# Kernel tuning notes

Measured on AMD Instinct MI355X. Metric: run time of the kernel, lower is better.

## Reference

```python
import jax, jax.numpy as jnp
import numpy as np

N, IN_DIM, OUT_DIM, HEADS, SUB = 4096, 256, 128, 4, 32
ETA = 0.5
LAMBDA_SPARSE = 0.05
NEG_BIG = -1e9


def setup_inputs() -> dict:
    key = jax.random.key(0)
    k1, k2, k3, k4 = jax.random.split(key, 4)
    H = jax.random.normal(k1, (N, IN_DIM), dtype=jnp.float32)
    # sparse binary adjacency mask (avg degree ~ 41) with self-loops
    adj_mask = (jax.random.uniform(k2, (N, N)) < 0.01).astype(jnp.float32)
    adj_mask = adj_mask.at[jnp.arange(N), jnp.arange(N)].set(1.0)
    # per-head orthonormal subspace bases U_k = QR(randn)[:, :SUB]
    raw = jax.random.normal(k3, (HEADS, IN_DIM, SUB), dtype=jnp.float32)
    U = jax.vmap(lambda r: jnp.linalg.qr(r)[0])(raw)  # [h, D, s]
    threshold = jnp.full((OUT_DIM,), LAMBDA_SPARSE, dtype=jnp.float32)
    proj_w = jax.random.normal(k4, (OUT_DIM, IN_DIM), dtype=jnp.float32) / np.float32(np.sqrt(IN_DIM))
    return {"H": H, "adj_mask": adj_mask, "U": U, "threshold": threshold, "proj_w": proj_w}


def reference(H, adj_mask, U, threshold, proj_w):
    # Z_k = U_k^T @ H^T  -> [h, s, N]
    Z = jnp.einsum('hds,nd->hsn', U, H)
    # scores_k = Z_k^T @ Z_k / sqrt(s)  -> [h, N, N]
    scores = jnp.einsum('hsn,hsm->hnm', Z, Z) / jnp.sqrt(jnp.float32(SUB))
    scores = scores + (1.0 - adj_mask)[None, :, :] * NEG_BIG
    alpha = jax.nn.softmax(scores, axis=-1)  # torch softmax(dim=1) on [N,N] rows
    # agg_k = Z_k @ alpha_k^T  -> [h, s, N];  sum_k U_k @ agg_k -> [D, N]
    agg = jnp.einsum('hsj,hij->hsi', Z, alpha)
    agg_sum = jnp.einsum('hds,hsn->dn', U, agg)
    H_half = H + ETA * agg_sum.T           # [N, D]
    H_half = H_half @ proj_w.T             # [N, out_dim]
    # soft-threshold
    H_out = jnp.sign(H_half) * jax.nn.relu(jnp.abs(H_half) - threshold[None, :])
    # orthogonality loss: sum_k ||U_k^T U_k - I||_F^2 + sum_{k<l} ||U_k^T U_l||_F^2
    G = jnp.einsum('kds,ldt->klst', U, U)  # [h, h, s, s]
    eye_s = jnp.eye(SUB, dtype=U.dtype)
    eye_h = jnp.eye(HEADS, dtype=U.dtype)
    sub = G - eye_h[:, :, None, None] * eye_s[None, None, :, :]
    sq = jnp.sum(sub ** 2, axis=(2, 3))    # [h, h]
    orth_loss = jnp.sum(jnp.triu(jnp.ones((HEADS, HEADS), dtype=U.dtype)) * sq)
    return H_out, orth_loss
```

## Files before the change

### kernel.cpp

```cpp
#include <hip/hip_runtime.h>
#include <hip/hip_bf16.h>
#include <math.h>

#define NN 4096
#define IN_DIM 256
#define OUT_DIM 128
#define HEADS 4
#define SUB 32
#define MAXDEG 128
#define ETA 0.5f
#define INV_SQRT_SUB 0.17677669529663687f

__global__ __launch_bounds__(256) void fused_small(const float* __restrict__ U,
                                                   const float* __restrict__ PW,
                                                   float* __restrict__ Wcomb,
                                                   float* __restrict__ W2,
                                                   float* __restrict__ loss) {
    int b = blockIdx.x;
    int t = threadIdx.x;
    __shared__ float sh[260];

    if (b < 256) {
        float v;
        if (b < 128) {
            int h = b >> 5, s = b & 31;
            v = U[h * IN_DIM * SUB + t * SUB + s];
        } else {
            v = PW[(b - 128) * IN_DIM + t];
        }
        Wcomb[b * IN_DIM + t] = v;
    } else if (b < 384) {
        int hs = b - 256;
        int h = hs >> 5, s = hs & 31;
        sh[t] = U[h * IN_DIM * SUB + t * SUB + s];
        __syncthreads();
        if (t < 128) {
            const float4* pw4 = (const float4*)(PW + t * IN_DIM);
            const float4* u4  = (const float4*)sh;
            float acc = 0.f;
            #pragma unroll 4
            for (int d4 = 0; d4 < 64; ++d4) {
                float4 a = u4[d4], p = pw4[d4];
                acc += a.x * p.x + a.y * p.y + a.z * p.z + a.w * p.w;
            }
            W2[hs * OUT_DIM + t] = acc;
        }
    } else {
        const int pk[10] = {0,0,0,0,1,1,1,2,2,3};
        const int pl[10] = {0,1,2,3,1,2,3,2,3,3};
        int p = b - 384;
        int k = pk[p], l = pl[p];
        int t2 = t & 31;
        int sg = t >> 5;
        const float* Uk = U + k * IN_DIM * SUB;
        const float* Ul = U + l * IN_DIM * SUB;
        float a0 = 0.f, a1 = 0.f, a2 = 0.f, a3 = 0.f;
        #pragma unroll 4
        for (int d = 0; d < IN_DIM; ++d) {
            float ul = Ul[d * SUB + t2];
            float u0 = Uk[d * SUB + sg * 4 + 0];
            float u1 = Uk[d * SUB + sg * 4 + 1];
            float u2 = Uk[d * SUB + sg * 4 + 2];
            float u3 = Uk[d * SUB + sg * 4 + 3];
            a0 += u0 * ul; a1 += u1 * ul; a2 += u2 * ul; a3 += u3 * ul;
        }
        if (k == l) {
            if (sg * 4 + 0 == t2) a0 -= 1.f;
            if (sg * 4 + 1 == t2) a1 -= 1.f;
            if (sg * 4 + 2 == t2) a2 -= 1.f;
            if (sg * 4 + 3 == t2) a3 -= 1.f;
        }
        float local = a0 * a0 + a1 * a1 + a2 * a2 + a3 * a3;
        local += __shfl_xor(local, 32, 64);
        local += __shfl_xor(local, 16, 64);
        local += __shfl_xor(local, 8, 64);
        local += __shfl_xor(local, 4, 64);
        local += __shfl_xor(local, 2, 64);
        local += __shfl_xor(local, 1, 64);
        if ((t & 63) == 0) sh[256 + (t >> 6)] = local;
        __syncthreads();
        if (t == 0) atomicAdd(loss, sh[256] + sh[257] + sh[258] + sh[259]);
    }
}

#define RPB 8
__global__ __launch_bounds__(256) void compute_zt_p(const float* __restrict__ H,
                                                    const float* __restrict__ Wcomb,
                                                    float* __restrict__ ZT,
                                                    float* __restrict__ P) {
    int t = threadIdx.x;
    int r0 = blockIdx.x * RPB;
    __shared__ float Hs[RPB][IN_DIM];
    const float4* H4 = (const float4*)(H + (size_t)r0 * IN_DIM);
    float4* Hs4 = (float4*)&Hs[0][0];
    Hs4[t]       = H4[t];
    Hs4[t + 256] = H4[t + 256];
    __syncthreads();

    float acc[RPB];
    #pragma unroll
    for (int r = 0; r < RPB; ++r) acc[r] = 0.f;

    const float4* Wr = (const float4*)(Wcomb + t * IN_DIM);
    float4 w = Wr[0];
    #pragma unroll 4
    for (int d4 = 0; d4 < 64; ++d4) {
        float4 wn = Wr[(d4 + 1 < 64) ? d4 + 1 : 63];
        #pragma unroll
        for (int r = 0; r < RPB; ++r) {
            float4 h = *(const float4*)&Hs[r][d4 * 4];
            acc[r] += h.x * w.x + h.y * w.y + h.z * w.z + h.w * w.w;
        }
        w = wn;
    }
    #pragma unroll
    for (int r = 0; r < RPB; ++r) {
        if (t < 128) ZT[(size_t)(r0 + r) * 128 + t] = acc[r];
        else         P [(size_t)(r0 + r) * 128 + (t - 128)] = acc[r];
    }
}

__global__ __launch_bounds__(128) void attn_core(const float* __restrict__ ZT,
                                                 const float* __restrict__ adj,
                                                 float* __restrict__ agg) {
    int i = blockIdx.x;
    int t = threadIdx.x;
    __shared__ int nbr_s[MAXDEG];
    __shared__ int cnt;
    if (t == 0) cnt = 0;
    __syncthreads();

    const float4* row4 = (const float4*)(adj + (size_t)i * NN);
    #pragma unroll
    for (int k2 = 0; k2 < NN / (128 * 4); ++k2) {
        float4 v = row4[t + k2 * 128];
        int j0 = (t + k2 * 128) * 4;
        if (v.x > 0.5f) { int p = atomicAdd(&cnt, 1); if (p < MAXDEG) nbr_s[p] = j0; }
        if (v.y > 0.5f) { int p = atomicAdd(&cnt, 1); if (p < MAXDEG) nbr_s[p] = j0 + 1; }
        if (v.z > 0.5f) { int p = atomicAdd(&cnt, 1); if (p < MAXDEG) nbr_s[p] = j0 + 2; }
        if (v.w > 0.5f) { int p = atomicAdd(&cnt, 1); if (p < MAXDEG) nbr_s[p] = j0 + 3; }
    }
    __syncthreads();
    int dg = cnt < MAXDEG ? cnt : MAXDEG;

    float q = ZT[(size_t)i * 128 + t];
    float accV = 0.f, accS = 0.f;

    for (int jj = 0; jj < dg; jj += 4) {
        int i0 = nbr_s[jj];
        int i1 = nbr_s[(jj + 1 < dg) ? jj + 1 : jj];
        int i2 = nbr_s[(jj + 2 < dg) ? jj + 2 : jj];
        int i3 = nbr_s[(jj + 3 < dg) ? jj + 3 : jj];
        float v0 = ZT[(size_t)i0 * 128 + t];
        float v1 = ZT[(size_t)i1 * 128 + t];
        float v2 = ZT[(size_t)i2 * 128 + t];
        float v3 = ZT[(size_t)i3 * 128 + t];
        float p0 = q * v0, p1 = q * v1, p2 = q * v2, p3 = q * v3;
        p0 += __shfl_xor(p0, 16, 32); p1 += __shfl_xor(p1, 16, 32);
        p2 += __shfl_xor(p2, 16, 32); p3 += __shfl_xor(p3, 16, 32);
        p0 += __shfl_xor(p0, 8, 32);  p1 += __shfl_xor(p1, 8, 32);
        p2 += __shfl_xor(p2, 8, 32);  p3 += __shfl_xor(p3, 8, 32);
        p0 += __shfl_xor(p0, 4, 32);  p1 += __shfl_xor(p1, 4, 32);
        p2 += __shfl_xor(p2, 4, 32);  p3 += __shfl_xor(p3, 4, 32);
        p0 += __shfl_xor(p0, 2, 32);  p1 += __shfl_xor(p1, 2, 32);
        p2 += __shfl_xor(p2, 2, 32);  p3 += __shfl_xor(p3, 2, 32);
        p0 += __shfl_xor(p0, 1, 32);  p1 += __shfl_xor(p1, 1, 32);
        p2 += __shfl_xor(p2, 1, 32);  p3 += __shfl_xor(p3, 1, 32);
        float e0 = __expf(p0 * INV_SQRT_SUB);
        float e1 = (jj + 1 < dg) ? __expf(p1 * INV_SQRT_SUB) : 0.f;
        float e2 = (jj + 2 < dg) ? __expf(p2 * INV_SQRT_SUB) : 0.f;
        float e3 = (jj + 3 < dg) ? __expf(p3 * INV_SQRT_SUB) : 0.f;
        accV += e0 * v0 + e1 * v1 + e2 * v2 + e3 * v3;
        accS += e0 + e1 + e2 + e3;
    }
    agg[(size_t)i * 128 + t] = accV * (ETA / accS);
}

#define EROWS 16
__global__ __launch_bounds__(256) void epilogue(const float* __restrict__ Pm,
                                                const float* __restrict__ agg,
                                                const float* __restrict__ W2,
                                                const float* __restrict__ threshold,
                                                float* __restrict__ out) {
    int t = threadIdx.x;
    int o = t & 127, half = t >> 7;
    int r0 = blockIdx.x * EROWS;
    __shared__ float As[EROWS][128];
    const float4* a4 = (const float4*)(agg + (size_t)r0 * 128);
    float4* As4 = (float4*)&As[0][0];
    As4[t]       = a4[t];
    As4[t + 256] = a4[t + 256];
    __syncthreads();

    float acc[8];
    #pragma unroll
    for (int r = 0; r < 8; ++r) acc[r] = 0.f;

    for (int q4 = 0; q4 < 32; ++q4) {
        int hs = q4 * 4;
        float w0 = W2[(hs + 0) * 128 + o];
        float w1 = W2[(hs + 1) * 128 + o];
        float w2v = W2[(hs + 2) * 128 + o];
        float w3 = W2[(hs + 3) * 128 + o];
        #pragma unroll
        for (int r = 0; r < 8; ++r) {
            float4 a = *(const float4*)&As[half * 8 + r][hs];
            acc[r] += a.x * w0 + a.y * w1 + a.z * w2v + a.w * w3;
        }
    }
    float th = threshold[o];
    #pragma unroll
    for (int r = 0; r < 8; ++r) {
        int row = r0 + half * 8 + r;
        float val = Pm[(size_t)row * 128 + o] + acc[r];
        float av = fabsf(val) - th;
        out[(size_t)row * 128 + o] = (av > 0.f) ? copysignf(av, val) : 0.f;
    }
}

extern "C" void kernel_launch(void* const* d_in, const int* in_sizes, int n_in,
                              void* d_out, int out_size, void* d_ws, size_t ws_size,
                              hipStream_t stream) {
    const float* H   = (const float*)d_in[0];
    const float* adj = (const float*)d_in[1];
    const float* U   = (const float*)d_in[2];
    const float* thr = (const float*)d_in[3];
    const float* PW  = (const float*)d_in[4];
    float* out = (float*)d_out;
    float* loss = out + (size_t)NN * OUT_DIM;

    char* ws = (char*)d_ws;
    float* ZT    = (float*)(ws);
    float* P     = (float*)(ws + (size_t)2097152);
    float* agg   = (float*)(ws + (size_t)4194304);
    float* W2    = (float*)(ws + (size_t)6291456);
    float* Wcomb = (float*)(ws + (size_t)6356992);

    hipMemsetAsync(loss, 0, sizeof(float), stream);
    fused_small<<<394, 256, 0, stream>>>(U, PW, Wcomb, W2, loss);
    compute_zt_p<<<NN / RPB, 256, 0, stream>>>(H, Wcomb, ZT, P);
    attn_core<<<NN, 128, 0, stream>>>(ZT, adj, agg);
    epilogue<<<NN / EROWS, 256, 0, stream>>>(P, agg, W2, thr, out);
}
```

Before: 169.6 us.

## Overlap adjacency scan with projection GEMM and fuse attention with epilogue

The adjacency-row scan now runs in its own blocks inside the front kernel, alongside the H@Wcomb projection, and writes neighbor lists and degrees to global memory. Attention and the output projection with soft-threshold are fused into one kernel. Per-neighbor, per-head scores are computed as dot products over float4 loads, replacing the shuffle reductions, and the loss is written as per-block partials instead of using a memset plus an atomic. This cuts the number of launches and the serial shuffle work in the gather loop. The cost is extra global traffic for the neighbor lists and a gather that now loads each neighbor row twice.

Result: slower. 221.9 us (+30.8%).

```diff
diff --git a/kernel.cpp b/kernel.cpp
--- a/kernel.cpp
+++ b/kernel.cpp
@@ -10,48 +10,41 @@
 #define MAXDEG 128
 #define ETA 0.5f
 #define INV_SQRT_SUB 0.17677669529663687f
-
-__global__ __launch_bounds__(256) void fused_small(const float* __restrict__ U,
-                                                   const float* __restrict__ PW,
-                                                   float* __restrict__ Wcomb,
-                                                   float* __restrict__ W2,
-                                                   float* __restrict__ loss) {
-    int b = blockIdx.x;
-    int t = threadIdx.x;
+#define SCAN_BLOCKS 2048
+#define RPB 8
+
+__global__ __launch_bounds__(256) void k_prep(const float* __restrict__ U,
+                                              const float* __restrict__ PW,
+                                              float* __restrict__ Wcomb,
+                                              float* __restrict__ W2T,
+                                              float* __restrict__ loss_parts) {
+    int b = blockIdx.x, t = threadIdx.x;
     __shared__ float sh[260];
-
     if (b < 256) {
         float v;
-        if (b < 128) {
-            int h = b >> 5, s = b & 31;
-            v = U[h * IN_DIM * SUB + t * SUB + s];
-        } else {
-            v = PW[(b - 128) * IN_DIM + t];
-        }
+        if (b < 128) { int h = b >> 5, s = b & 31; v = U[h * IN_DIM * SUB + t * SUB + s]; }
+        else          v = PW[(b - 128) * IN_DIM + t];
         Wcomb[b * IN_DIM + t] = v;
     } else if (b < 384) {
-        int hs = b - 256;
-        int h = hs >> 5, s = hs & 31;
+        int hs = b - 256, h = hs >> 5, s = hs & 31;
         sh[t] = U[h * IN_DIM * SUB + t * SUB + s];
         __syncthreads();
         if (t < 128) {
             const float4* pw4 = (const float4*)(PW + t * IN_DIM);
             const float4* u4  = (const float4*)sh;
             float acc = 0.f;
-            #pragma unroll 4
+            #pragma unroll 8
             for (int d4 = 0; d4 < 64; ++d4) {
                 float4 a = u4[d4], p = pw4[d4];
                 acc += a.x * p.x + a.y * p.y + a.z * p.z + a.w * p.w;
             }
-            W2[hs * OUT_DIM + t] = acc;
+            W2T[t * OUT_DIM + hs] = acc;
         }
     } else {
         const int pk[10] = {0,0,0,0,1,1,1,2,2,3};
         const int pl[10] = {0,1,2,3,1,2,3,2,3,3};
-        int p = b - 384;
-        int k = pk[p], l = pl[p];
-        int t2 = t & 31;
-        int sg = t >> 5;
+        int p = b - 384, k = pk[p], l = pl[p];
+        int t2 = t & 31, sg = t >> 5;
         const float* Uk = U + k * IN_DIM * SUB;
         const float* Ul = U + l * IN_DIM * SUB;
         float a0 = 0.f, a1 = 0.f, a2 = 0.f, a3 = 0.f;
@@ -79,143 +72,139 @@
         local += __shfl_xor(local, 1, 64);
         if ((t & 63) == 0) sh[256 + (t >> 6)] = local;
         __syncthreads();
-        if (t == 0) atomicAdd(loss, sh[256] + sh[257] + sh[258] + sh[259]);
-    }
-}
-
-#define RPB 8
-__global__ __launch_bounds__(256) void compute_zt_p(const float* __restrict__ H,
-                                                    const float* __restrict__ Wcomb,
-                                                    float* __restrict__ ZT,
-                                                    float* __restrict__ P) {
-    int t = threadIdx.x;
-    int r0 = blockIdx.x * RPB;
+        if (t == 0) loss_parts[p] = sh[256] + sh[257] + sh[258] + sh[259];
+    }
+}
+
+__global__ __launch_bounds__(256) void k_front(const float* __restrict__ H,
+                                               const float* __restrict__ adj,
+                                               const float* __restrict__ Wcomb,
+                                               float* __restrict__ ZT,
+                                               float* __restrict__ P,
+                                               int* __restrict__ nbr,
+                                               int* __restrict__ deg) {
+    int b = blockIdx.x, t = threadIdx.x;
     __shared__ float Hs[RPB][IN_DIM];
-    const float4* H4 = (const float4*)(H + (size_t)r0 * IN_DIM);
-    float4* Hs4 = (float4*)&Hs[0][0];
-    Hs4[t]       = H4[t];
-    Hs4[t + 256] = H4[t + 256];
+    __shared__ int cnt[2];
+    if (b < SCAN_BLOCKS) {
+        int half = t >> 7, u = t & 127;
+        int row = b * 2 + half;
+        if (u == 0) cnt[half] = 0;
+        __syncthreads();
+        const float4* row4 = (const float4*)(adj + (size_t)row * NN);
+        int* nrow = nbr + row * MAXDEG;
+        #pragma unroll
+        for (int k = 0; k < NN / (128 * 4); ++k) {
+            float4 v = row4[u + k * 128];
+            int j0 = (u + k * 128) * 4;
+            if (v.x > 0.5f) { int p = atomicAdd(&cnt[half], 1); if (p < MAXDEG) nrow[p] = j0; }
+            if (v.y > 0.5f) { int p = atomicAdd(&cnt[half], 1); if (p < MAXDEG) nrow[p] = j0 + 1; }
+            if (v.z > 0.5f) { int p = atomicAdd(&cnt[half], 1); if (p < MAXDEG) nrow[p] = j0 + 2; }
+            if (v.w > 0.5f) { int p = atomicAdd(&cnt[half], 1); if (p < MAXDEG) nrow[p] = j0 + 3; }
+        }
+        __syncthreads();
+        if (u == 0) deg[row] = cnt[half] < MAXDEG ? cnt[half] : MAXDEG;
+    } else {
+        int r0 = (b - SCAN_BLOCKS) * RPB;
+        const float4* H4 = (const float4*)(H + (size_t)r0 * IN_DIM);
+        float4* Hs4 = (float4*)&Hs[0][0];
+        Hs4[t]       = H4[t];
+        Hs4[t + 256] = H4[t + 256];
+        __syncthreads();
+        float acc[RPB];
+        #pragma unroll
+        for (int r = 0; r < RPB; ++r) acc[r] = 0.f;
+        const float4* Wr = (const float4*)(Wcomb + t * IN_DIM);
+        #pragma unroll 4
+        for (int d4 = 0; d4 < 64; ++d4) {
+            float4 w = Wr[d4];
+            #pragma unroll
+            for (int r = 0; r < RPB; ++r) {
+                float4 h = *(const float4*)&Hs[r][d4 * 4];
+                acc[r] += h.x * w.x + h.y * w.y + h.z * w.z + h.w * w.w;
+            }
+        }
+        #pragma unroll
+        for (int r = 0; r < RPB; ++r) {
+            if (t < 128) ZT[(size_t)(r0 + r) * 128 + t] = acc[r];
+            else         P [(size_t)(r0 + r) * 128 + (t - 128)] = acc[r];
+        }
+    }
+}
+
+__global__ __launch_bounds__(256) void k_attn(const float* __restrict__ ZT,
+                                              const float* __restrict__ Pm,
+                                              const float* __restrict__ W2T,
+                                              const int* __restrict__ nbr,
+                                              const int* __restrict__ deg,
+                                              const float* __restrict__ threshold,
+                                              const float* __restrict__ loss_parts,
+                                              float* __restrict__ out) {
+    int b = blockIdx.x, t = threadIdx.x;
+    int half = t >> 7, u = t & 127;
+    int row = b * 2 + half;
+    __shared__ float z_s[2][128];
+    __shared__ float e_s[2][MAXDEG][HEADS];
+    __shared__ int   nbr_s[2][MAXDEG];
+    __shared__ float agg_s[2][128];
+
+    if (b == 0 && t == 0) {
+        float L = 0.f;
+        #pragma unroll
+        for (int p = 0; p < 10; ++p) L += loss_parts[p];
+        out[(size_t)NN * OUT_DIM] = L;
+    }
+
+    int dgv = deg[row];
+    z_s[half][u] = ZT[(size_t)row * 128 + u];
+    nbr_s[half][u] = (u < dgv) ? nbr[row * MAXDEG + u] : 0;
     __syncthreads();
 
-    float acc[RPB];
-    #pragma unroll
-    for (int r = 0; r < RPB; ++r) acc[r] = 0.f;
-
-    const float4* Wr = (const float4*)(Wcomb + t * IN_DIM);
-    float4 w = Wr[0];
-    #pragma unroll 4
-    for (int d4 = 0; d4 < 64; ++d4) {
-        float4 wn = Wr[(d4 + 1 < 64) ? d4 + 1 : 63];
-        #pragma unroll
-        for (int r = 0; r < RPB; ++r) {
-            float4 h = *(const float4*)&Hs[r][d4 * 4];
-            acc[r] += h.x * w.x + h.y * w.y + h.z * w.z + h.w * w.w;
-        }
-        w = wn;
-    }
-    #pragma unroll
-    for (int r = 0; r < RPB; ++r) {
-        if (t < 128) ZT[(size_t)(r0 + r) * 128 + t] = acc[r];
-        else         P [(size_t)(r0 + r) * 128 + (t - 128)] = acc[r];
-    }
-}
-
-__global__ __launch_bounds__(128) void attn_core(const float* __restrict__ ZT,
-                                                 const float* __restrict__ adj,
-                                                 float* __restrict__ agg) {
-    int i = blockIdx.x;
-    int t = threadIdx.x;
-    __shared__ int nbr_s[MAXDEG];
-    __shared__ int cnt;
-    if (t == 0) cnt = 0;
+    int jj0 = u >> 2, h = u & 3;
+    int ntiles = (dgv + 31) >> 5;
+    const float4* qr = (const float4*)(&z_s[half][h * 32]);
+    for (int tile = 0; tile < ntiles; ++tile) {
+        int jj = tile * 32 + jj0;
+        int j = nbr_s[half][jj];
+        const float4* zr = (const float4*)(ZT + (size_t)j * 128 + h * 32);
+        float acc = 0.f;
+        #pragma unroll
+        for (int k = 0; k < 8; ++k) {
+            float4 z = zr[k];
+            float4 q = qr[k];
+            acc += z.x * q.x + z.y * q.y + z.z * q.z + z.w * q.w;
+        }
+        e_s[half][jj][h] = (jj < dgv) ? __expf(acc * INV_SQRT_SUB) : 0.f;
+    }
     __syncthreads();
 
-    const float4* row4 = (const float4*)(adj + (size_t)i * NN);
-    #pragma unroll
-    for (int k2 = 0; k2 < NN / (128 * 4); ++k2) {
-        float4 v = row4[t + k2 * 128];
-        int j0 = (t + k2 * 128) * 4;
-        if (v.x > 0.5f) { int p = atomicAdd(&cnt, 1); if (p < MAXDEG) nbr_s[p] = j0; }
-        if (v.y > 0.5f) { int p = atomicAdd(&cnt, 1); if (p < MAXDEG) nbr_s[p] = j0 + 1; }
-        if (v.z > 0.5f) { int p = atomicAdd(&cnt, 1); if (p < MAXDEG) nbr_s[p] = j0 + 2; }
-        if (v.w > 0.5f) { int p = atomicAdd(&cnt, 1); if (p < MAXDEG) nbr_s[p] = j0 + 3; }
-    }
+    int hh = u >> 5;
+    float accV = 0.f, accS = 0.f;
+    const float* zbase = ZT + u;
+    for (int jj = 0; jj < dgv; jj += 4) {
+        int ja = nbr_s[half][jj],     jb = nbr_s[half][jj + 1];
+        int jc = nbr_s[half][jj + 2], jd = nbr_s[half][jj + 3];
+        float ea = e_s[half][jj][hh],     eb = e_s[half][jj + 1][hh];
+        float ec = e_s[half][jj + 2][hh], ed = e_s[half][jj + 3][hh];
+        float va = zbase[(size_t)ja * 128], vb = zbase[(size_t)jb * 128];
+        float vc = zbase[(size_t)jc * 128], vd = zbase[(size_t)jd * 128];
+        accV += ea * va + eb * vb + ec * vc + ed * vd;
+        accS += (ea + eb) + (ec + ed);
+    }
+    agg_s[half][u] = accV * (ETA / accS);
     __syncthreads();
-    int dg = cnt < MAXDEG ? cnt : MAXDEG;
-
-    float q = ZT[(size_t)i * 128 + t];
-    float accV = 0.f, accS = 0.f;
-
-    for (int jj = 0; jj < dg; jj += 4) {
-        int i0 = nbr_s[jj];
-        int i1 = nbr_s[(jj + 1 < dg) ? jj + 1 : jj];
-        int i2 = nbr_s[(jj + 2 < dg) ? jj + 2 : jj];
-        int i3 = nbr_s[(jj + 3 < dg) ? jj + 3 : jj];
-        float v0 = ZT[(size_t)i0 * 128 + t];
-        float v1 = ZT[(size_t)i1 * 128 + t];
-        float v2 = ZT[(size_t)i2 * 128 + t];
-        float v3 = ZT[(size_t)i3 * 128 + t];
-        float p0 = q * v0, p1 = q * v1, p2 = q * v2, p3 = q * v3;
-        p0 += __shfl_xor(p0, 16, 32); p1 += __shfl_xor(p1, 16, 32);
-        p2 += __shfl_xor(p2, 16, 32); p3 += __shfl_xor(p3, 16, 32);
-        p0 += __shfl_xor(p0, 8, 32);  p1 += __shfl_xor(p1, 8, 32);
-        p2 += __shfl_xor(p2, 8, 32);  p3 += __shfl_xor(p3, 8, 32);
-        p0 += __shfl_xor(p0, 4, 32);  p1 += __shfl_xor(p1, 4, 32);
-        p2 += __shfl_xor(p2, 4, 32);  p3 += __shfl_xor(p3, 4, 32);
-        p0 += __shfl_xor(p0, 2, 32);  p1 += __shfl_xor(p1, 2, 32);
-        p2 += __shfl_xor(p2, 2, 32);  p3 += __shfl_xor(p3, 2, 32);
-        p0 += __shfl_xor(p0, 1, 32);  p1 += __shfl_xor(p1, 1, 32);
-        p2 += __shfl_xor(p2, 1, 32);  p3 += __shfl_xor(p3, 1, 32);
-        float e0 = __expf(p0 * INV_SQRT_SUB);
-        float e1 = (jj + 1 < dg) ? __expf(p1 * INV_SQRT_SUB) : 0.f;
-        float e2 = (jj + 2 < dg) ? __expf(p2 * INV_SQRT_SUB) : 0.f;
-        float e3 = (jj + 3 < dg) ? __expf(p3 * INV_SQRT_SUB) : 0.f;
-        accV += e0 * v0 + e1 * v1 + e2 * v2 + e3 * v3;
-        accS += e0 + e1 + e2 + e3;
-    }
-    agg[(size_t)i * 128 + t] = accV * (ETA / accS);
-}
-
-#define EROWS 16
-__global__ __launch_bounds__(256) void epilogue(const float* __restrict__ Pm,
-                                                const float* __restrict__ agg,
-                                                const float* __restrict__ W2,
-                                                const float* __restrict__ threshold,
-                                                float* __restrict__ out) {
-    int t = threadIdx.x;
-    int o = t & 127, half = t >> 7;
-    int r0 = blockIdx.x * EROWS;
-    __shared__ float As[EROWS][128];
-    const float4* a4 = (const float4*)(agg + (size_t)r0 * 128);
-    float4* As4 = (float4*)&As[0][0];
-    As4[t]       = a4[t];
-    As4[t + 256] = a4[t + 256];
-    __syncthreads();
-
-    float acc[8];
-    #pragma unroll
-    for (int r = 0; r < 8; ++r) acc[r] = 0.f;
-
-    for (int q4 = 0; q4 < 32; ++q4) {
-        int hs = q4 * 4;
-        float w0 = W2[(hs + 0) * 128 + o];
-        float w1 = W2[(hs + 1) * 128 + o];
-        float w2v = W2[(hs + 2) * 128 + o];
-        float w3 = W2[(hs + 3) * 128 + o];
-        #pragma unroll
-        for (int r = 0; r < 8; ++r) {
-            float4 a = *(const float4*)&As[half * 8 + r][hs];
-            acc[r] += a.x * w0 + a.y * w1 + a.z * w2v + a.w * w3;
-        }
-    }
-    float th = threshold[o];
-    #pragma unroll
-    for (int r = 0; r < 8; ++r) {
-        int row = r0 + half * 8 + r;
-        float val = Pm[(size_t)row * 128 + o] + acc[r];
-        float av = fabsf(val) - th;
-        out[(size_t)row * 128 + o] = (av > 0.f) ? copysignf(av, val) : 0.f;
-    }
+
+    float val = Pm[(size_t)row * 128 + u];
+    const float4* w4 = (const float4*)(W2T + u * 128);
+    const float4* a4 = (const float4*)(&agg_s[half][0]);
+    #pragma unroll 8
+    for (int k = 0; k < 32; ++k) {
+        float4 w = w4[k], a = a4[k];
+        val += w.x * a.x + w.y * a.y + w.z * a.z + w.w * a.w;
+    }
+    float th = threshold[u];
+    float av = fabsf(val) - th;
+    out[(size_t)row * 128 + u] = (av > 0.f) ? copysignf(av, val) : 0.f;
 }
 
 extern "C" void kernel_launch(void* const* d_in, const int* in_sizes, int n_in,
@@ -227,18 +216,17 @@
     const float* thr = (const float*)d_in[3];
     const float* PW  = (const float*)d_in[4];
     float* out = (float*)d_out;
-    float* loss = out + (size_t)NN * OUT_DIM;
 
     char* ws = (char*)d_ws;
     float* ZT    = (float*)(ws);
     float* P     = (float*)(ws + (size_t)2097152);
-    float* agg   = (float*)(ws + (size_t)4194304);
-    float* W2    = (float*)(ws + (size_t)6291456);
-    float* Wcomb = (float*)(ws + (size_t)6356992);
-
-    hipMemsetAsync(loss, 0, sizeof(float), stream);
-    fused_small<<<394, 256, 0, stream>>>(U, PW, Wcomb, W2, loss);
-    compute_zt_p<<<NN / RPB, 256, 0, stream>>>(H, Wcomb, ZT, P);
-    attn_core<<<NN, 128, 0, stream>>>(ZT, adj, agg);
-    epilogue<<<NN / EROWS, 256, 0, stream>>>(P, agg, W2, thr, out);
-}
+    float* Wcomb = (float*)(ws + (size_t)4194304);
+    float* W2T   = (float*)(ws + (size_t)4456448);
+    int*   nbr   = (int*)  (ws + (size_t)4521984);
+    int*   deg   = (int*)  (ws + (size_t)6619136);
+    float* lossp = (float*)(ws + (size_t)6635520);
+
+    k_prep<<<394, 256, 0, stream>>>(U, PW, Wcomb, W2T, lossp);
+    k_front<<<SCAN_BLOCKS + NN / RPB, 256, 0, stream>>>(H, adj, Wcomb, ZT, P, nbr, deg);
+    k_attn<<<NN / 2, 256, 0, stream>>>(ZT, P, W2T, nbr, deg, thr, lossp, out);
+}
```

## Restructure attention scores into per-thread head dot products staged in shared memory

Applied to the files above, without the earlier changes.

Changes attn_core so the adjacency row loads are all issued up front before the neighbour compaction. Scores are now computed by assigning each thread one (neighbour, head) pair that does a 32-wide dot product from shared-memory q, and the exponentials are stored in shared memory. The aggregation loop then only gathers values and accumulates, removing the shuffle-reduction chains. compute_zt_p halves rows per block to launch more blocks and prefetches weights two steps ahead. This costs more shared memory and an extra barrier, and it gathers ZT twice.

Result: slower. 176.2 us (+3.9%).

```diff
diff --git a/kernel.cpp b/kernel.cpp
--- a/kernel.cpp
+++ b/kernel.cpp
@@ -83,7 +83,7 @@
     }
 }
 
-#define RPB 8
+#define RPB 4
 __global__ __launch_bounds__(256) void compute_zt_p(const float* __restrict__ H,
                                                     const float* __restrict__ Wcomb,
                                                     float* __restrict__ ZT,
@@ -92,9 +92,7 @@
     int r0 = blockIdx.x * RPB;
     __shared__ float Hs[RPB][IN_DIM];
     const float4* H4 = (const float4*)(H + (size_t)r0 * IN_DIM);
-    float4* Hs4 = (float4*)&Hs[0][0];
-    Hs4[t]       = H4[t];
-    Hs4[t + 256] = H4[t + 256];
+    ((float4*)&Hs[0][0])[t] = H4[t];
     __syncthreads();
 
     float acc[RPB];
@@ -102,16 +100,16 @@
     for (int r = 0; r < RPB; ++r) acc[r] = 0.f;
 
     const float4* Wr = (const float4*)(Wcomb + t * IN_DIM);
-    float4 w = Wr[0];
+    float4 w0 = Wr[0], w1 = Wr[1];
     #pragma unroll 4
     for (int d4 = 0; d4 < 64; ++d4) {
-        float4 wn = Wr[(d4 + 1 < 64) ? d4 + 1 : 63];
+        float4 wn = Wr[(d4 + 2 < 64) ? d4 + 2 : 63];
+        float4 w = w0; w0 = w1; w1 = wn;
         #pragma unroll
         for (int r = 0; r < RPB; ++r) {
             float4 h = *(const float4*)&Hs[r][d4 * 4];
             acc[r] += h.x * w.x + h.y * w.y + h.z * w.z + h.w * w.w;
         }
-        w = wn;
     }
     #pragma unroll
     for (int r = 0; r < RPB; ++r) {
@@ -125,53 +123,62 @@
                                                  float* __restrict__ agg) {
     int i = blockIdx.x;
     int t = threadIdx.x;
-    __shared__ int nbr_s[MAXDEG];
+    __shared__ int   nbr_s[MAXDEG];
+    __shared__ float e_s[MAXDEG][HEADS];
+    __shared__ float z_s[128];
     __shared__ int cnt;
+
+    const float4* row4 = (const float4*)(adj + (size_t)i * NN);
+    float4 v[8];
+    #pragma unroll
+    for (int k = 0; k < 8; ++k) v[k] = row4[t + k * 128];
+
     if (t == 0) cnt = 0;
-    __syncthreads();
-
-    const float4* row4 = (const float4*)(adj + (size_t)i * NN);
-    #pragma unroll
-    for (int k2 = 0; k2 < NN / (128 * 4); ++k2) {
-        float4 v = row4[t + k2 * 128];
-        int j0 = (t + k2 * 128) * 4;
-        if (v.x > 0.5f) { int p = atomicAdd(&cnt, 1); if (p < MAXDEG) nbr_s[p] = j0; }
-        if (v.y > 0.5f) { int p = atomicAdd(&cnt, 1); if (p < MAXDEG) nbr_s[p] = j0 + 1; }
-        if (v.z > 0.5f) { int p = atomicAdd(&cnt, 1); if (p < MAXDEG) nbr_s[p] = j0 + 2; }
-        if (v.w > 0.5f) { int p = atomicAdd(&cnt, 1); if (p < MAXDEG) nbr_s[p] = j0 + 3; }
+    nbr_s[t] = 0;
+    z_s[t] = ZT[(size_t)i * 128 + t];
+    __syncthreads();
+
+    #pragma unroll
+    for (int k = 0; k < 8; ++k) {
+        int j0 = (t + k * 128) * 4;
+        if (v[k].x > 0.5f) { int p = atomicAdd(&cnt, 1); if (p < MAXDEG) nbr_s[p] = j0; }
+        if (v[k].y > 0.5f) { int p = atomicAdd(&cnt, 1); if (p < MAXDEG) nbr_s[p] = j0 + 1; }
+        if (v[k].z > 0.5f) { int p = atomicAdd(&cnt, 1); if (p < MAXDEG) nbr_s[p] = j0 + 2; }
+        if (v[k].w > 0.5f) { int p = atomicAdd(&cnt, 1); if (p < MAXDEG) nbr_s[p] = j0 + 3; }
     }
     __syncthreads();
     int dg = cnt < MAXDEG ? cnt : MAXDEG;
 
-    float q = ZT[(size_t)i * 128 + t];
+    int jj0 = t >> 2, h = t & 3;
+    int ntiles = (dg + 31) >> 5;
+    const float4* qr = (const float4*)(&z_s[h * 32]);
+    for (int tile = 0; tile < ntiles; ++tile) {
+        int jj = tile * 32 + jj0;
+        int j = nbr_s[jj];
+        const float4* zr = (const float4*)(ZT + (size_t)j * 128 + h * 32);
+        float acc = 0.f;
+        #pragma unroll
+        for (int k = 0; k < 8; ++k) {
+            float4 z = zr[k];
+            float4 q = qr[k];
+            acc += z.x * q.x + z.y * q.y + z.z * q.z + z.w * q.w;
+        }
+        e_s[jj][h] = (jj < dg) ? __expf(acc * INV_SQRT_SUB) : 0.f;
+    }
+    __syncthreads();
+
+    int hh = t >> 5;
     float accV = 0.f, accS = 0.f;
-
+    const float* zbase = ZT + t;
     for (int jj = 0; jj < dg; jj += 4) {
-        int i0 = nbr_s[jj];
-        int i1 = nbr_s[(jj + 1 < dg) ? jj + 1 : jj];
-        int i2 = nbr_s[(jj + 2 < dg) ? jj + 2 : jj];
-        int i3 = nbr_s[(jj + 3 < dg) ? jj + 3 : jj];
-        float v0 = ZT[(size_t)i0 * 128 + t];
-        float v1 = ZT[(size_t)i1 * 128 + t];
-        float v2 = ZT[(size_t)i2 * 128 + t];
-        float v3 = ZT[(size_t)i3 * 128 + t];
-        float p0 = q * v0, p1 = q * v1, p2 = q * v2, p3 = q * v3;
-        p0 += __shfl_xor(p0, 16, 32); p1 += __shfl_xor(p1, 16, 32);
-        p2 += __shfl_xor(p2, 16, 32); p3 += __shfl_xor(p3, 16, 32);
-        p0 += __shfl_xor(p0, 8, 32);  p1 += __shfl_xor(p1, 8, 32);
-        p2 += __shfl_xor(p2, 8, 32);  p3 += __shfl_xor(p3, 8, 32);
-        p0 += __shfl_xor(p0, 4, 32);  p1 += __shfl_xor(p1, 4, 32);
-        p2 += __shfl_xor(p2, 4, 32);  p3 += __shfl_xor(p3, 4, 32);
-        p0 += __shfl_xor(p0, 2, 32);  p1 += __shfl_xor(p1, 2, 32);
-        p2 += __shfl_xor(p2, 2, 32);  p3 += __shfl_xor(p3, 2, 32);
-        p0 += __shfl_xor(p0, 1, 32);  p1 += __shfl_xor(p1, 1, 32);
-        p2 += __shfl_xor(p2, 1, 32);  p3 += __shfl_xor(p3, 1, 32);
-        float e0 = __expf(p0 * INV_SQRT_SUB);
-        float e1 = (jj + 1 < dg) ? __expf(p1 * INV_SQRT_SUB) : 0.f;
-        float e2 = (jj + 2 < dg) ? __expf(p2 * INV_SQRT_SUB) : 0.f;
-        float e3 = (jj + 3 < dg) ? __expf(p3 * INV_SQRT_SUB) : 0.f;
-        accV += e0 * v0 + e1 * v1 + e2 * v2 + e3 * v3;
-        accS += e0 + e1 + e2 + e3;
+        int ja = nbr_s[jj],     jb = nbr_s[jj + 1];
+        int jc = nbr_s[jj + 2], jd = nbr_s[jj + 3];
+        float ea = e_s[jj][hh],     eb = e_s[jj + 1][hh];
+        float ec = e_s[jj + 2][hh], ed = e_s[jj + 3][hh];
+        float va = zbase[(size_t)ja * 128], vb = zbase[(size_t)jb * 128];
+        float vc = zbase[(size_t)jc * 128], vd = zbase[(size_t)jd * 128];
+        accV += ea * va + eb * vb + ec * vc + ed * vd;
+        accS += (ea + eb) + (ec + ed);
     }
     agg[(size_t)i * 128 + t] = accV * (ETA / accS);
 }
```
